# Performance work log

Measured on AMD Instinct MI355X. Metric: run time of the kernel, lower is better.

## Reference

```python
import jax, jax.numpy as jnp
import numpy as np

VOCAB, EMB, HID = 50000, 128, 256
B, T = 64, 512


def setup_inputs() -> dict:
    key = jax.random.key(0)
    ks = jax.random.split(key, 10)
    node = jax.random.randint(ks[0], (B, T, 2), 0, VOCAB, dtype=jnp.int32)
    rel = jax.random.randint(ks[1], (B, T, 3), 0, VOCAB, dtype=jnp.int32)
    father = jax.random.randint(ks[2], (B, T), 0, T, dtype=jnp.int32)
    mask = jnp.ones((B, T), jnp.float32)
    # parameters (PyTorch LSTM layout: gates ordered i,f,g,o)
    embedding = jax.random.normal(ks[3], (VOCAB, EMB), jnp.float32) * 1e-4
    W_ih = jax.random.uniform(ks[4], (4 * HID, 2 * EMB), jnp.float32, -0.02, 0.02)
    W_hh = jax.random.uniform(ks[5], (4 * HID, HID), jnp.float32, -0.02, 0.02)
    b_ih = jnp.zeros((4 * HID,), jnp.float32).at[HID:2 * HID].set(1.0)  # forget bias = 1
    b_hh = jnp.zeros((4 * HID,), jnp.float32)
    W_h = jax.random.normal(ks[6], (HID, HID), jnp.float32) * 0.02
    return {"src_gtr_seq_node": node, "src_gtr_seq_rel": rel,
            "src_gtr_seq_father": father, "src_gtr_seq_node_mask": mask,
            "embedding": embedding, "W_ih": W_ih, "W_hh": W_hh,
            "b_ih": b_ih, "b_hh": b_hh, "W_h": W_h}


def reference(src_gtr_seq_node, src_gtr_seq_rel, src_gtr_seq_father,
              src_gtr_seq_node_mask, embedding, W_ih, W_hh, b_ih, b_hh, W_h):
    node, rel, father, mask = (src_gtr_seq_node, src_gtr_seq_rel,
                               src_gtr_seq_father, src_gtr_seq_node_mask)
    Bn, Tn = node.shape[:2]
    H = W_hh.shape[1]
    t_idx = jnp.arange(Tn, dtype=jnp.int32)
    # valid parent at step t must point into memory slots [0..t]; -1 -> zero root slot
    father = jnp.minimum(father, (t_idx - 1)[None, :])
    # 'avg' mode: mean of first-2 node token embeddings, mean of rel token embeddings
    node_e = embedding[node].mean(axis=2)            # [B,T,E]
    rel_e = embedding[rel].mean(axis=2)              # [B,T,E]
    x = jnp.concatenate([node_e, rel_e], axis=-1)    # [B,T,2E]
    gx = jnp.einsum('bte,ge->btg', x, W_ih) + b_ih   # [B,T,4H] input-side gates
    barange = jnp.arange(Bn)
    h_mem0 = jnp.zeros((Tn + 1, Bn, H), x.dtype)     # slot 0 = zero state (root)
    c_mem0 = jnp.zeros((Tn + 1, Bn, H), x.dtype)

    def step(carry, inp):
        h_mem, c_mem = carry
        t, gx_t, f_t = inp
        h_prev = h_mem[f_t + 1, barange]             # parent gather [B,H]
        c_prev = c_mem[f_t + 1, barange]
        gates = gx_t + h_prev @ W_hh.T + b_hh        # [B,4H]
        i, f, g, o = jnp.split(gates, 4, axis=-1)
        c = jax.nn.sigmoid(f) * c_prev + jax.nn.sigmoid(i) * jnp.tanh(g)
        h = jax.nn.sigmoid(o) * jnp.tanh(c)
        return (h_mem.at[t + 1].set(h), c_mem.at[t + 1].set(c)), h

    (h_mem, c_mem), outs = jax.lax.scan(
        step, (h_mem0, c_mem0),
        (t_idx, gx.transpose(1, 0, 2), father.T))
    m = mask[:, :, None]
    encoder_outputs = outs.transpose(1, 0, 2) * m    # [B,T,H]
    encoder_feature = encoder_outputs.reshape(-1, H) @ W_h.T  # [B*T,H]
    h_max = (h_mem[1:].transpose(1, 0, 2) * m).max(axis=1)[None]  # [1,B,H]
    c_max = (c_mem[1:].transpose(1, 0, 2) * m).max(axis=1)[None]
    return encoder_outputs, encoder_feature, h_max, c_max
```

## Files before the change

kernel.cpp:

```cpp
#include <hip/hip_runtime.h>
#include <hip/hip_bf16.h>
#include <math.h>

#define NB 64
#define NT 512
#define NH 256
#define NG 1024

typedef __bf16 bf16x8 __attribute__((ext_vector_type(8)));
typedef float  f32x4  __attribute__((ext_vector_type(4)));

static __device__ __forceinline__ unsigned short f2bf(float x){
  __hip_bfloat16 h = __float2bfloat16(x);
  return __builtin_bit_cast(unsigned short, h);
}
static __device__ __forceinline__ float bf2f(unsigned short u){
  return __bfloat162float(__builtin_bit_cast(__hip_bfloat16, u));
}

#if __has_builtin(__builtin_amdgcn_sdot4)
#define SDOT4(a,b,c) __builtin_amdgcn_sdot4((a),(b),(c),false)
#else
static __device__ __forceinline__ int SDOT4(int a, int b, int c){
  c += ((a<<24)>>24)*((b<<24)>>24);
  c += ((a<<16)>>24)*((b<<16)>>24);
  c += ((a<< 8)>>24)*((b<< 8)>>24);
  c += ( a     >>24)*( b     >>24);
  return c;
}
#endif

#define BAR_LGKM() asm volatile("s_waitcnt lgkmcnt(0)\n\ts_barrier" ::: "memory")
#define BAR_ALL()  asm volatile("s_waitcnt vmcnt(0) lgkmcnt(0)\n\ts_barrier" ::: "memory")

#define PIN(x) asm volatile("" : "+v"(x))

static __device__ __forceinline__ float tanh_acc(float x){
  float ax = fabsf(x);
  if (ax < 0.04f){
    float x2 = x*x;
    return x * (1.0f + x2*(-(1.0f/3.0f) + x2*(2.0f/15.0f)));
  }
  float e = __expf(-2.0f*ax);
  float r = (1.0f - e) / (1.0f + e);
  return copysignf(r, x);
}
static __device__ __forceinline__ float sigm(float x){
  return 1.0f / (1.0f + __expf(-x));
}

#define HSCALE 1270000.0f
#define WSCALE 6350.0f
#define DQ_CONST (1.0f/(HSCALE*WSCALE))

__global__ __launch_bounds__(256) void k_prep(
    const float* __restrict__ Wih, const float* __restrict__ Whh,
    const float* __restrict__ Wh,  const float* __restrict__ bih,
    const float* __restrict__ bhh,
    unsigned short* __restrict__ wih_bf, unsigned short* __restrict__ wh_bf,
    int* __restrict__ wq, float* __restrict__ bias)
{
  int i = blockIdx.x*256 + threadIdx.x;
  wih_bf[i] = f2bf(Wih[i]);
  if (i < 65536){
    wh_bf[i] = f2bf(Wh[i]);
    float4 wv = *(const float4*)(Whh + (long)i*4);
    int q0 = (int)rintf(wv.x * WSCALE); q0 = max(-127, min(127, q0));
    int q1 = (int)rintf(wv.y * WSCALE); q1 = max(-127, min(127, q1));
    int q2 = (int)rintf(wv.z * WSCALE); q2 = max(-127, min(127, q2));
    int q3 = (int)rintf(wv.w * WSCALE); q3 = max(-127, min(127, q3));
    wq[i] = (q0&255) | ((q1&255)<<8) | ((q2&255)<<16) | ((q3&255)<<24);
  }
  if (i < 1024) bias[i] = bih[i] + bhh[i];
}

__global__ __launch_bounds__(128) void k_x(
    const int* __restrict__ node, const int* __restrict__ rel,
    const float* __restrict__ emb, unsigned short* __restrict__ x)
{
  int bt = blockIdx.x; int e = threadIdx.x;
  int n0 = node[bt*2+0], n1 = node[bt*2+1];
  int r0 = rel[bt*3+0], r1 = rel[bt*3+1], r2 = rel[bt*3+2];
  float a = (emb[(long)n0*128+e] + emb[(long)n1*128+e]) * 0.5f;
  float b = (emb[(long)r0*128+e] + emb[(long)r1*128+e] + emb[(long)r2*128+e]) * (1.0f/3.0f);
  x[(long)bt*256 + e]       = f2bf(a);
  x[(long)bt*256 + 128 + e] = f2bf(b);
}

__global__ __launch_bounds__(256) void k_gemm(
    const unsigned short* __restrict__ A, const unsigned short* __restrict__ Bw,
    unsigned short* __restrict__ Cbf, float* __restrict__ Cf32,
    const float* __restrict__ mask, int N, int mode)
{
  __shared__ __align__(16) unsigned short As[64][32];
  __shared__ __align__(16) unsigned short Bs[64][32];
  const int tid = threadIdx.x;
  const int lane = tid & 63, wave = tid >> 6;
  const int wm = wave >> 1, wn = wave & 1;
  const int l15 = lane & 15, quad = lane >> 4;
  const int tM = blockIdx.x * 64, tN = blockIdx.y * 64;
  const int srow = tid >> 2, sseg = tid & 3;
  f32x4 acc[2][2] = {};
  long arow = tM + srow;
  if (mode == 1) arow = arow + (arow >> 9) + 1;
  const unsigned short* Aptr = A + arow*256 + sseg*8;
  const unsigned short* Bptr = Bw + (long)(tN + srow)*256 + sseg*8;
  for (int kc = 0; kc < 8; ++kc){
    bf16x8 av = *(const bf16x8*)(Aptr + kc*32);
    bf16x8 bv = *(const bf16x8*)(Bptr + kc*32);
    *(bf16x8*)&As[srow][sseg*8] = av;
    *(bf16x8*)&Bs[srow][sseg*8] = bv;
    __syncthreads();
    bf16x8 af[2], bg[2];
    #pragma unroll
    for (int i=0;i<2;++i) af[i] = *(const bf16x8*)&As[wm*32 + i*16 + l15][quad*8];
    #pragma unroll
    for (int j=0;j<2;++j) bg[j] = *(const bf16x8*)&Bs[wn*32 + j*16 + l15][quad*8];
    #pragma unroll
    for (int i=0;i<2;++i)
      #pragma unroll
      for (int j=0;j<2;++j)
        acc[i][j] = __builtin_amdgcn_mfma_f32_16x16x32_bf16(af[i], bg[j], acc[i][j], 0,0,0);
    __syncthreads();
  }
  #pragma unroll
  for (int i=0;i<2;++i)
  #pragma unroll
  for (int j=0;j<2;++j)
  #pragma unroll
  for (int r=0;r<4;++r){
    int m = tM + wm*32 + i*16 + quad*4 + r;
    int n = tN + wn*32 + j*16 + l15;
    float v = acc[i][j][r];
    if (mode == 0) Cbf[(long)m*N + n] = f2bf(v);
    else           Cf32[(long)m*N + n] = v * mask[m];
  }
}

__global__ __launch_bounds__(512, 2) void k_scan(
    const int* __restrict__ father, const unsigned short* __restrict__ gx,
    const int* __restrict__ wq_g, const float* __restrict__ bias,
    unsigned short* __restrict__ h_hist, float* __restrict__ c_hist)
{
  const int b    = blockIdx.x;
  const int tid  = threadIdx.x;
  const int lane = tid & 63;
  const int wave = tid >> 6;
  const int half = lane >> 5;
  const int u    = wave*32 + (lane & 31);
  extern __shared__ int smem[];
  int* hqh  = smem;
  int* fbuf = smem + 513*64;

  const int rowA = half*256 + u;
  const int rowB = rowA + 512;

  int wA[64], wB[64];
  {
    const int4* pA = (const int4*)(wq_g + (long)rowA*64);
    const int4* pB = (const int4*)(wq_g + (long)rowB*64);
    #pragma unroll
    for (int j=0;j<16;++j){
      int4 a = pA[j], c = pB[j];
      wA[4*j+0]=a.x; wA[4*j+1]=a.y; wA[4*j+2]=a.z; wA[4*j+3]=a.w;
      wB[4*j+0]=c.x; wB[4*j+1]=c.y; wB[4*j+2]=c.z; wB[4*j+3]=c.w;
    }
  }
  #pragma unroll
  for (int j=0;j<64;++j){ PIN(wA[j]); PIN(wB[j]); }

  const float bA = bias[rowA];
  const float bB = bias[rowB];
  fbuf[tid] = father[b*512 + tid];
  if (tid < 64) hqh[tid] = 0;

  const unsigned short* gxp = gx + (long)b*524288;
  unsigned int ga0 = gxp[rowA];
  unsigned int gb0 = gxp[rowB];
  unsigned int ga1 = gxp[1024 + rowA];
  unsigned int gb1 = gxp[1024 + rowB];
  const unsigned short* gptr = gxp + 2*1024 + rowA;
  unsigned short* hst = h_hist + ((long)b*513 + 1)*256 + u;
  float*          cst = c_hist + ((long)b*513 + 1)*256 + u;
  const char*     clb = (const char*)(c_hist + (long)b*513*256 + u);

  float cpl0 = 0.f, cpl1 = 0.f;
  float cm1 = 0.f, cm2 = 0.f, cm3 = 0.f;
  float selv = 0.f; int useL = 0;
  int hbase = 0;
  int lastBar = -1;
  BAR_ALL();
  int fc1 = fbuf[1];

#define SCAN_BODY(T, CPL, GA, GB)                                              \
  {                                                                            \
    const int t = (T);                                                         \
                                       \
    int a0a=0,a0b=0,a1a=0,a1b=0;                                               \
    _Pragma("unroll")                                                          \
    for (int kc = 0; kc < 8; ++kc){                                            \
      int4 h0 = *(const int4*)&hqh[hbase + kc*8];                              \
      int4 h1 = *(const int4*)&hqh[hbase + kc*8 + 4];                          \
      a0a = SDOT4(wA[8*kc+0], h0.x, a0a); a1a = SDOT4(wB[8*kc+0], h0.x, a1a);  \
      a0a = SDOT4(wA[8*kc+1], h0.y, a0a); a1a = SDOT4(wB[8*kc+1], h0.y, a1a);  \
      a0a = SDOT4(wA[8*kc+2], h0.z, a0a); a1a = SDOT4(wB[8*kc+2], h0.z, a1a);  \
      a0a = SDOT4(wA[8*kc+3], h0.w, a0a); a1a = SDOT4(wB[8*kc+3], h0.w, a1a);  \
      a0b = SDOT4(wA[8*kc+4], h1.x, a0b); a1b = SDOT4(wB[8*kc+4], h1.x, a1b);  \
      a0b = SDOT4(wA[8*kc+5], h1.y, a0b); a1b = SDOT4(wB[8*kc+5], h1.y, a1b);  \
      a0b = SDOT4(wA[8*kc+6], h1.z, a0b); a1b = SDOT4(wB[8*kc+6], h1.z, a1b);  \
      a0b = SDOT4(wA[8*kc+7], h1.w, a0b); a1b = SDOT4(wB[8*kc+7], h1.w, a1b);  \
    }                                                                          \
    int a0 = a0a + a0b, a1 = a1a + a1b;                                        \
             \
    asm volatile("s_waitcnt vmcnt(5)" : "+v"(CPL), "+v"(GA), "+v"(GB));        \
    float gAf = __uint_as_float(GA << 16);                                     \
    float gBf = __uint_as_float(GB << 16);                                     \
    float vA = (float)a0 * DQ_CONST + gAf + bA;                                \
    float vB = (float)a1 * DQ_CONST + gBf + bB;                                \
                 \
    float s0 = sigm(vA);                                \
    float th = tanh_acc(vB);                            \
    float s1 = sigm(vB);                                \
    float sf = __shfl_xor(s0, 32, 64);                                         \
    float so = __shfl_xor(s1, 32, 64);                                         \
    float pre = s0 * th;                                                       \
    float cp  = useL ? CPL : selv;                                             \
    float c   = fmaf(sf, cp, pre);                                             \
    float h   = so * tanh_acc(c);               \
    if (lane < 32){                                                            \
      unsigned int hb = (unsigned int)f2bf(h);                                 \
      asm volatile("global_store_short %0, %1, off" :: "v"(hst), "v"(hb));     \
      asm volatile("global_store_dword %0, %1, off" :: "v"(cst), "v"(c));      \
      int q = (int)rintf(h * HSCALE);                                          \
      q = max(-127, min(127, q));                                              \
      ((char*)hqh)[(t+1)*256 + u] = (char)q;                                   \
    }                                                                          \
    cm3 = cm2; cm2 = cm1; cm1 = c;                                             \
    hst += 256; cst += 256;                                                    \
     \
    int fr2 = __builtin_amdgcn_readfirstlane(fbuf[t+2 < 512 ? t+2 : 511]);     \
    {                                                                          \
      int fL = min(fr2, t+1);                                                  \
      const char* cla = clb + (long)(fL+1)*1024;                               \
      asm volatile("global_load_dword %0, %1, off" : "=v"(CPL) : "v"(cla));    \
      asm volatile("global_load_ushort %0, %1, off" : "=v"(GA) : "v"(gptr));   \
      asm volatile("global_load_ushort %0, %1, off offset:1024"                \
                   : "=v"(GB) : "v"(gptr));                                    \
    }                                                                          \
    if (t < 509) gptr += 1024;                                                 \
            \
    {                                                                          \
      int fA = min(fc1, t);                                                    \
      useL = (fA < t-2);                                                       \
      selv = (fA == t) ? cm1 : ((fA == t-1) ? cm2 : cm3);                      \
      hbase = (fA + 1) * 64;                                                   \
      fc1 = fr2;                                                               \
      if (fA > lastBar){                                                       \
        BAR_LGKM();                                                            \
        lastBar = t;                                                           \
      }                                                                        \
    }                                                                          \
  }

  #pragma unroll 1
  for (int tb = 0; tb < 512; tb += 2){
    SCAN_BODY(tb,   cpl0, ga0, gb0)
    SCAN_BODY(tb+1, cpl1, ga1, gb1)
  }
#undef SCAN_BODY
}

__global__ __launch_bounds__(256) void k_eo1(
    const unsigned short* __restrict__ h_hist, const float* __restrict__ c_hist,
    const float* __restrict__ mask, float* __restrict__ out,
    float* __restrict__ pmax)
{
  int b = blockIdx.x, s = blockIdx.y, tid = threadIdx.x;
  float hm = -INFINITY, cm = -INFINITY;
  for (int i=0; i<64; ++i){
    int t = s*64 + i;
    long off = ((long)b*513 + t + 1)*256 + tid;
    float h = bf2f(h_hist[off]);
    float c = c_hist[off];
    float m = mask[b*512 + t];
    float e = h*m;
    out[((long)b*512 + t)*256 + tid] = e;
    hm = fmaxf(hm, e);
    cm = fmaxf(cm, c*m);
  }
  long po = ((long)(b*8 + s))*512 + tid;
  pmax[po]       = hm;
  pmax[po + 256] = cm;
}

__global__ __launch_bounds__(256) void k_eo2(
    const float* __restrict__ pmax, float* __restrict__ out)
{
  int b = blockIdx.x, tid = threadIdx.x;
  float hm = -INFINITY, cm = -INFINITY;
  for (int s=0; s<8; ++s){
    long po = ((long)(b*8 + s))*512 + tid;
    hm = fmaxf(hm, pmax[po]);
    cm = fmaxf(cm, pmax[po + 256]);
  }
  out[16777216L + b*256 + tid] = hm;
  out[16793600L + b*256 + tid] = cm;
}

extern "C" void kernel_launch(void* const* d_in, const int* in_sizes, int n_in,
                              void* d_out, int out_size, void* d_ws, size_t ws_size,
                              hipStream_t stream)
{
  const int*   node   = (const int*)  d_in[0];
  const int*   rel    = (const int*)  d_in[1];
  const int*   father = (const int*)  d_in[2];
  const float* mask   = (const float*)d_in[3];
  const float* emb    = (const float*)d_in[4];
  const float* Wih    = (const float*)d_in[5];
  const float* Whh    = (const float*)d_in[6];
  const float* bih    = (const float*)d_in[7];
  const float* bhh    = (const float*)d_in[8];
  const float* Wh     = (const float*)d_in[9];

  char* ws = (char*)d_ws;
  unsigned short* x_bf   = (unsigned short*)(ws);
  unsigned short* h_hist = (unsigned short*)(ws + 16777216);
  float*          c_hist = (float*)         (ws + 33587200);
  unsigned short* wih_bf = (unsigned short*)(ws + 75612160);
  unsigned short* wh_bf  = (unsigned short*)(ws + 76136448);
  int*            wq     = (int*)           (ws + 76267520);
  float*          bias   = (float*)         (ws + 76529664);
  float*          pmax   = (float*)(ws);

  unsigned short* gxbuf = (unsigned short*)d_out;
  float* out = (float*)d_out;

  const int scan_lds = (513*64 + 512)*4;

  k_prep<<<1024, 256, 0, stream>>>(Wih, Whh, Wh, bih, bhh, wih_bf, wh_bf, wq, bias);
  k_x<<<32768, 128, 0, stream>>>(node, rel, emb, x_bf);
  k_gemm<<<dim3(512,16), 256, 0, stream>>>(x_bf, wih_bf, gxbuf, nullptr, nullptr, 1024, 0);
  k_scan<<<64, 512, scan_lds, stream>>>(father, gxbuf, wq, bias, h_hist, c_hist);
  k_gemm<<<dim3(512,4), 256, 0, stream>>>(h_hist, wh_bf, nullptr, out + 8388608, mask, 256, 1);
  k_eo1<<<dim3(64,8), 256, 0, stream>>>(h_hist, c_hist, mask, out, pmax);
  k_eo2<<<64, 256, 0, stream>>>(pmax, out);
}
```

Measured before the change: 714.9 us.

## Split recurrent dot product across 4 lanes with DPP reduction and gate-interleaved gx

Restructures the scan so each group of 4 lanes covers two hidden units across all four gates. Each lane does a quarter of the K dimension for 8 rows, and the partial sums are combined with DPP adds. Weights are repacked in the prep kernel to match, and the gx GEMM output is stored gate-interleaved so one dwordx2 load fetches all four gate inputs. This removes the cross-half shuffles and cuts the per-step LDS reads of h. In exchange it adds DPP reduction steps, redundant activation math on the duplicate lanes, and uses 128 weight registers, with launch bounds dropped to one block per SM.

```diff
diff --git a/kernel.cpp b/kernel.cpp
--- a/kernel.cpp
+++ b/kernel.cpp
@@ -9,6 +9,7 @@
 
 typedef __bf16 bf16x8 __attribute__((ext_vector_type(8)));
 typedef float  f32x4  __attribute__((ext_vector_type(4)));
+typedef unsigned int u32x2 __attribute__((ext_vector_type(2)));
 
 static __device__ __forceinline__ unsigned short f2bf(float x){
   __hip_bfloat16 h = __float2bfloat16(x);
@@ -30,6 +31,11 @@
 }
 #endif
 
+#define QRED(x) do {                                                      \
+    x += __builtin_amdgcn_update_dpp(0, x, 0xB1, 0xF, 0xF, true);         \
+    x += __builtin_amdgcn_update_dpp(0, x, 0x4E, 0xF, 0xF, true);         \
+  } while(0)
+
 #define BAR_LGKM() asm volatile("s_waitcnt lgkmcnt(0)\n\ts_barrier" ::: "memory")
 #define BAR_ALL()  asm volatile("s_waitcnt vmcnt(0) lgkmcnt(0)\n\ts_barrier" ::: "memory")
 
@@ -69,7 +75,15 @@
     int q1 = (int)rintf(wv.y * WSCALE); q1 = max(-127, min(127, q1));
     int q2 = (int)rintf(wv.z * WSCALE); q2 = max(-127, min(127, q2));
     int q3 = (int)rintf(wv.w * WSCALE); q3 = max(-127, min(127, q3));
-    wq[i] = (q0&255) | ((q1&255)<<8) | ((q2&255)<<16) | ((q3&255)<<24);
+    int packed = (q0&255) | ((q1&255)<<8) | ((q2&255)<<16) | ((q3&255)<<24);
+    int R = i >> 6, j = i & 63;
+    int gate = R >> 8, ug = R & 255;
+    int wv_ = ug >> 5, ul = ug & 31;
+    int grp = ul >> 1, s = ul & 1;
+    int ck = j >> 4, k = j & 15;
+    int lane2 = grp*4 + ck;
+    int r = gate*2 + s;
+    wq[(((long)wv_*64 + lane2)*8 + r)*16 + k] = packed;
   }
   if (i < 1024) bias[i] = bih[i] + bhh[i];
 }
@@ -132,12 +146,12 @@
     int m = tM + wm*32 + i*16 + quad*4 + r;
     int n = tN + wn*32 + j*16 + l15;
     float v = acc[i][j][r];
-    if (mode == 0) Cbf[(long)m*N + n] = f2bf(v);
+    if (mode == 0) Cbf[(long)m*1024 + ((n&255)<<2) + (n>>8)] = f2bf(v);
     else           Cf32[(long)m*N + n] = v * mask[m];
   }
 }
 
-__global__ __launch_bounds__(512, 2) void k_scan(
+__global__ __launch_bounds__(512, 1) void k_scan(
     const int* __restrict__ father, const unsigned short* __restrict__ gx,
     const int* __restrict__ wq_g, const float* __restrict__ bias,
     unsigned short* __restrict__ h_hist, float* __restrict__ c_hist)
@@ -146,40 +160,38 @@
   const int tid  = threadIdx.x;
   const int lane = tid & 63;
   const int wave = tid >> 6;
-  const int half = lane >> 5;
-  const int u    = wave*32 + (lane & 31);
+  const int c4   = lane & 3;
+  const int g16  = lane >> 2;
+  const int s    = c4 & 1;
+  const int u    = wave*32 + g16*2 + s;
+  const int wrt  = (c4 < 2);
   extern __shared__ int smem[];
   int* hqh  = smem;
   int* fbuf = smem + 513*64;
 
-  const int rowA = half*256 + u;
-  const int rowB = rowA + 512;
-
-  int wA[64], wB[64];
+  int w[128];
   {
-    const int4* pA = (const int4*)(wq_g + (long)rowA*64);
-    const int4* pB = (const int4*)(wq_g + (long)rowB*64);
+    const int4* p = (const int4*)(wq_g + ((long)(wave*64 + lane))*128);
     #pragma unroll
-    for (int j=0;j<16;++j){
-      int4 a = pA[j], c = pB[j];
-      wA[4*j+0]=a.x; wA[4*j+1]=a.y; wA[4*j+2]=a.z; wA[4*j+3]=a.w;
-      wB[4*j+0]=c.x; wB[4*j+1]=c.y; wB[4*j+2]=c.z; wB[4*j+3]=c.w;
+    for (int j=0;j<32;++j){
+      int4 v = p[j];
+      w[4*j+0]=v.x; w[4*j+1]=v.y; w[4*j+2]=v.z; w[4*j+3]=v.w;
     }
   }
   #pragma unroll
-  for (int j=0;j<64;++j){ PIN(wA[j]); PIN(wB[j]); }
-
-  const float bA = bias[rowA];
-  const float bB = bias[rowB];
+  for (int j=0;j<128;++j) PIN(w[j]);
+
+  const float bI = bias[u];
+  const float bF = bias[256+u];
+  const float bG = bias[512+u];
+  const float bO = bias[768+u];
   fbuf[tid] = father[b*512 + tid];
   if (tid < 64) hqh[tid] = 0;
 
   const unsigned short* gxp = gx + (long)b*524288;
-  unsigned int ga0 = gxp[rowA];
-  unsigned int gb0 = gxp[rowB];
-  unsigned int ga1 = gxp[1024 + rowA];
-  unsigned int gb1 = gxp[1024 + rowB];
-  const unsigned short* gptr = gxp + 2*1024 + rowA;
+  u32x2 gv0 = *(const u32x2*)(gxp + (long)u*4);
+  u32x2 gv1 = *(const u32x2*)(gxp + 1024 + (long)u*4);
+  const unsigned short* gptr = gxp + 2*1024 + u*4;
   unsigned short* hst = h_hist + ((long)b*513 + 1)*256 + u;
   float*          cst = c_hist + ((long)b*513 + 1)*256 + u;
   const char*     clb = (const char*)(c_hist + (long)b*513*256 + u);
@@ -192,60 +204,71 @@
   BAR_ALL();
   int fc1 = fbuf[1];
 
-#define SCAN_BODY(T, CPL, GA, GB)                                              \
+#define SCAN_BODY(T, CPL, GXV)                                                 \
   {                                                                            \
     const int t = (T);                                                         \
-                                       \
-    int a0a=0,a0b=0,a1a=0,a1b=0;                                               \
+         \
+    int4 ha = *(const int4*)&hqh[hbase + c4*16 + 0];                           \
+    int4 hb = *(const int4*)&hqh[hbase + c4*16 + 4];                           \
+    int4 hc = *(const int4*)&hqh[hbase + c4*16 + 8];                           \
+    int4 hd = *(const int4*)&hqh[hbase + c4*16 + 12];                          \
+    int acc[8] = {0,0,0,0,0,0,0,0};                                            \
     _Pragma("unroll")                                                          \
-    for (int kc = 0; kc < 8; ++kc){                                            \
-      int4 h0 = *(const int4*)&hqh[hbase + kc*8];                              \
-      int4 h1 = *(const int4*)&hqh[hbase + kc*8 + 4];                          \
-      a0a = SDOT4(wA[8*kc+0], h0.x, a0a); a1a = SDOT4(wB[8*kc+0], h0.x, a1a);  \
-      a0a = SDOT4(wA[8*kc+1], h0.y, a0a); a1a = SDOT4(wB[8*kc+1], h0.y, a1a);  \
-      a0a = SDOT4(wA[8*kc+2], h0.z, a0a); a1a = SDOT4(wB[8*kc+2], h0.z, a1a);  \
-      a0a = SDOT4(wA[8*kc+3], h0.w, a0a); a1a = SDOT4(wB[8*kc+3], h0.w, a1a);  \
-      a0b = SDOT4(wA[8*kc+4], h1.x, a0b); a1b = SDOT4(wB[8*kc+4], h1.x, a1b);  \
-      a0b = SDOT4(wA[8*kc+5], h1.y, a0b); a1b = SDOT4(wB[8*kc+5], h1.y, a1b);  \
-      a0b = SDOT4(wA[8*kc+6], h1.z, a0b); a1b = SDOT4(wB[8*kc+6], h1.z, a1b);  \
-      a0b = SDOT4(wA[8*kc+7], h1.w, a0b); a1b = SDOT4(wB[8*kc+7], h1.w, a1b);  \
+    for (int r=0;r<8;++r){                                                     \
+      acc[r] = SDOT4(w[r*16+ 0], ha.x, acc[r]);                                \
+      acc[r] = SDOT4(w[r*16+ 1], ha.y, acc[r]);                                \
+      acc[r] = SDOT4(w[r*16+ 2], ha.z, acc[r]);                                \
+      acc[r] = SDOT4(w[r*16+ 3], ha.w, acc[r]);                                \
+      acc[r] = SDOT4(w[r*16+ 4], hb.x, acc[r]);                                \
+      acc[r] = SDOT4(w[r*16+ 5], hb.y, acc[r]);                                \
+      acc[r] = SDOT4(w[r*16+ 6], hb.z, acc[r]);                                \
+      acc[r] = SDOT4(w[r*16+ 7], hb.w, acc[r]);                                \
+      acc[r] = SDOT4(w[r*16+ 8], hc.x, acc[r]);                                \
+      acc[r] = SDOT4(w[r*16+ 9], hc.y, acc[r]);                                \
+      acc[r] = SDOT4(w[r*16+10], hc.z, acc[r]);                                \
+      acc[r] = SDOT4(w[r*16+11], hc.w, acc[r]);                                \
+      acc[r] = SDOT4(w[r*16+12], hd.x, acc[r]);                                \
+      acc[r] = SDOT4(w[r*16+13], hd.y, acc[r]);                                \
+      acc[r] = SDOT4(w[r*16+14], hd.z, acc[r]);                                \
+      acc[r] = SDOT4(w[r*16+15], hd.w, acc[r]);                                \
     }                                                                          \
-    int a0 = a0a + a0b, a1 = a1a + a1b;                                        \
-             \
-    asm volatile("s_waitcnt vmcnt(5)" : "+v"(CPL), "+v"(GA), "+v"(GB));        \
-    float gAf = __uint_as_float(GA << 16);                                     \
-    float gBf = __uint_as_float(GB << 16);                                     \
-    float vA = (float)a0 * DQ_CONST + gAf + bA;                                \
-    float vB = (float)a1 * DQ_CONST + gBf + bB;                                \
-                 \
-    float s0 = sigm(vA);                                \
-    float th = tanh_acc(vB);                            \
-    float s1 = sigm(vB);                                \
-    float sf = __shfl_xor(s0, 32, 64);                                         \
-    float so = __shfl_xor(s1, 32, 64);                                         \
-    float pre = s0 * th;                                                       \
+            \
+    _Pragma("unroll")                                                          \
+    for (int r=0;r<8;++r) QRED(acc[r]);                                        \
+                  \
+    asm volatile("s_waitcnt vmcnt(4)" : "+v"(CPL), "+v"(GXV));                 \
+    float xi = __uint_as_float(GXV.x << 16);                                   \
+    float xf = __uint_as_float(GXV.x & 0xFFFF0000u);                           \
+    float xg = __uint_as_float(GXV.y << 16);                                   \
+    float xo = __uint_as_float(GXV.y & 0xFFFF0000u);                           \
+    int ai = s ? acc[1] : acc[0];                                              \
+    int af = s ? acc[3] : acc[2];                                              \
+    int ag = s ? acc[5] : acc[4];                                              \
+    int ao = s ? acc[7] : acc[6];                                              \
+    float vi = (float)ai * DQ_CONST + xi + bI;                                 \
+    float vf = (float)af * DQ_CONST + xf + bF;                                 \
+    float vg = (float)ag * DQ_CONST + xg + bG;                                 \
+    float vo = (float)ao * DQ_CONST + xo + bO;                                 \
     float cp  = useL ? CPL : selv;                                             \
-    float c   = fmaf(sf, cp, pre);                                             \
-    float h   = so * tanh_acc(c);               \
-    if (lane < 32){                                                            \
-      unsigned int hb = (unsigned int)f2bf(h);                                 \
-      asm volatile("global_store_short %0, %1, off" :: "v"(hst), "v"(hb));     \
-      asm volatile("global_store_dword %0, %1, off" :: "v"(cst), "v"(c));      \
-      int q = (int)rintf(h * HSCALE);                                          \
+    float cc_ = fmaf(sigm(vf), cp, sigm(vi)*tanh_acc(vg));                     \
+    float hh_ = sigm(vo)*tanh_acc(cc_);                                        \
+    if (wrt){                                                                  \
+      unsigned int hb16 = (unsigned int)f2bf(hh_);                             \
+      asm volatile("global_store_short %0, %1, off" :: "v"(hst), "v"(hb16));   \
+      asm volatile("global_store_dword %0, %1, off" :: "v"(cst), "v"(cc_));    \
+      int q = (int)rintf(hh_ * HSCALE);                                        \
       q = max(-127, min(127, q));                                              \
       ((char*)hqh)[(t+1)*256 + u] = (char)q;                                   \
     }                                                                          \
-    cm3 = cm2; cm2 = cm1; cm1 = c;                                             \
+    cm3 = cm2; cm2 = cm1; cm1 = cc_;                                           \
     hst += 256; cst += 256;                                                    \
-     \
+              \
     int fr2 = __builtin_amdgcn_readfirstlane(fbuf[t+2 < 512 ? t+2 : 511]);     \
     {                                                                          \
       int fL = min(fr2, t+1);                                                  \
       const char* cla = clb + (long)(fL+1)*1024;                               \
       asm volatile("global_load_dword %0, %1, off" : "=v"(CPL) : "v"(cla));    \
-      asm volatile("global_load_ushort %0, %1, off" : "=v"(GA) : "v"(gptr));   \
-      asm volatile("global_load_ushort %0, %1, off offset:1024"                \
-                   : "=v"(GB) : "v"(gptr));                                    \
+      asm volatile("global_load_dwordx2 %0, %1, off" : "=v"(GXV) : "v"(gptr)); \
     }                                                                          \
     if (t < 509) gptr += 1024;                                                 \
             \
@@ -264,8 +287,8 @@
 
   #pragma unroll 1
   for (int tb = 0; tb < 512; tb += 2){
-    SCAN_BODY(tb,   cpl0, ga0, gb0)
-    SCAN_BODY(tb+1, cpl1, ga1, gb1)
+    SCAN_BODY(tb,   cpl0, gv0)
+    SCAN_BODY(tb+1, cpl1, gv1)
   }
 #undef SCAN_BODY
 }
```

Result: slower. 779.1 us (+9.0%).
